# Performance work log

Hardware: AMD Instinct MI355X
Metric: run time of the kernel (lower is better)

## Reference

```python
import jax, jax.numpy as jnp
import numpy as np

B, S, D = 4, 2048, 1024
H, DK = 16, 64
NUM_BUCKETS = 32
MAX_DISTANCE = 128
EPS = 1e-6


def _relative_position_bucket(q_len, kv_len):
    # causal (bidirectional=False) T5 bucketization
    ctx = jnp.arange(q_len, dtype=jnp.int32)[:, None]
    mem = jnp.arange(kv_len, dtype=jnp.int32)[None, :]
    rp = mem - ctx                       # [q, kv]
    rp = -jnp.minimum(rp, 0)             # nonnegative distances to the past
    max_exact = NUM_BUCKETS // 2
    is_small = rp < max_exact
    rp_safe = jnp.maximum(rp, 1).astype(jnp.float32)
    large = max_exact + (
        jnp.log(rp_safe / max_exact) / np.log(MAX_DISTANCE / max_exact) * (NUM_BUCKETS - max_exact)
    ).astype(jnp.int32)
    large = jnp.minimum(large, NUM_BUCKETS - 1)
    return jnp.where(is_small, rp, large)  # [q, kv] int32 in [0, NUM_BUCKETS)


def setup_inputs() -> dict:
    key = jax.random.key(0)
    k1, k2, k3, k4 = jax.random.split(key, 4)
    hidden_states = jax.random.normal(k1, (B, S, D), dtype=jnp.float32)
    sequence_mask = jnp.ones((B, S), dtype=bool)
    rms_w = jnp.ones((D,), dtype=jnp.float32)
    W_qkv = jax.random.normal(k2, (D, 3 * H * DK), dtype=jnp.float32) * (D ** -0.5)
    W_o = jax.random.normal(k3, (H * DK, D), dtype=jnp.float32) * ((H * DK) ** -0.5)
    rel_bias = jax.random.normal(k4, (NUM_BUCKETS, H), dtype=jnp.float32)
    return {"hidden_states": hidden_states, "sequence_mask": sequence_mask,
            "rms_w": rms_w, "W_qkv": W_qkv, "W_o": W_o, "rel_bias": rel_bias}


def reference(hidden_states, sequence_mask, rms_w, W_qkv, W_o, rel_bias):
    # RMSNorm
    var = jnp.mean(hidden_states * hidden_states, axis=-1, keepdims=True)
    normed = hidden_states * jax.lax.rsqrt(var + EPS) * rms_w

    # QKV projection -> [B, S, 3, H, DK] -> [B, H, S, DK] each
    qkv = (normed @ W_qkv).reshape(B, S, 3, H, DK)
    q = jnp.transpose(qkv[:, :, 0], (0, 2, 1, 3))
    k = jnp.transpose(qkv[:, :, 1], (0, 2, 1, 3))
    v = jnp.transpose(qkv[:, :, 2], (0, 2, 1, 3))

    # relative position bias: gather [S,S,H] -> [1,H,S,S]
    bucket = _relative_position_bucket(S, S)
    pos_bias = jnp.transpose(rel_bias[bucket], (2, 0, 1))[None]

    # scores (note: T5 does NOT scale by 1/sqrt(dk))
    scores = jnp.einsum("bhqd,bhkd->bhqk", q, k) + pos_bias

    # causal mask combined with sequence mask (True = attend)
    causal = jnp.tril(jnp.ones((S, S), dtype=bool))
    mask = causal[None, None] & sequence_mask[:, None, None, :]
    scores = jnp.where(mask, scores, jnp.finfo(scores.dtype).min)

    attn = jax.nn.softmax(scores.astype(jnp.float32), axis=-1).astype(scores.dtype)
    # dropout p=0 / eval mode -> identity
    ctx = jnp.einsum("bhqk,bhkd->bhqd", attn, v)          # [B,H,S,DK]
    ctx = jnp.transpose(ctx, (0, 2, 1, 3)).reshape(B, S, H * DK)
    out = hidden_states + ctx @ W_o                        # residual
    return out
```

## Files before the change

### kernel.cpp

```cpp
#include <hip/hip_runtime.h>
#include <math.h>


typedef unsigned short ushort_t;
typedef __attribute__((ext_vector_type(8))) short bfrag;
typedef __attribute__((ext_vector_type(4))) float ffrag;

#define MFMA16(a, b, c) __builtin_amdgcn_mfma_f32_16x16x32_bf16((a), (b), (c), 0, 0, 0)

__device__ __forceinline__ void load_lds16(const ushort_t* g, ushort_t* l) {
  __builtin_amdgcn_global_load_lds(
      (const __attribute__((address_space(1))) unsigned int*)g,
      (__attribute__((address_space(3))) unsigned int*)l, 16, 0, 0);
}

__device__ __forceinline__ ushort_t f2bf(float f) {
  union { float f; unsigned u; } x; x.f = f;
  unsigned r = x.u + 0x7FFFu + ((x.u >> 16) & 1u);
  return (ushort_t)(r >> 16);
}
__device__ __forceinline__ float bf2f(ushort_t u) {
  union { unsigned u; float f; } x; x.u = ((unsigned)u) << 16; return x.f;
}
__device__ __forceinline__ unsigned pk2bf(float lo, float hi) {
  union { float f; unsigned u; } a, b; a.f = lo; b.f = hi;
  unsigned ra = a.u + 0x7FFFu + ((a.u >> 16) & 1u);
  unsigned rb = b.u + 0x7FFFu + ((b.u >> 16) & 1u);
  return (ra >> 16) | (rb & 0xFFFF0000u);
}

__global__ __launch_bounds__(256) void norm_cvt_kernel(
    const float* __restrict__ hidden, const float* __restrict__ rms_w,
    ushort_t* __restrict__ normed) {
  const int w = threadIdx.x >> 6, lane = threadIdx.x & 63;
  const int row = blockIdx.x * 4 + w;
  const float* p = hidden + (size_t)row * 1024;
  float4 v[4];
  float s = 0.f;
#pragma unroll
  for (int i = 0; i < 4; ++i) {
    v[i] = *(const float4*)(p + (lane + i * 64) * 4);
    s += v[i].x * v[i].x + v[i].y * v[i].y + v[i].z * v[i].z + v[i].w * v[i].w;
  }
#pragma unroll
  for (int off = 1; off < 64; off <<= 1) s += __shfl_xor(s, off, 64);
  const float scale = rsqrtf(s * (1.0f / 1024.0f) + 1e-6f);
#pragma unroll
  for (int i = 0; i < 4; ++i) {
    const int c0 = (lane + i * 64) * 4;
    float4 wv = *(const float4*)(rms_w + c0);
    ushort4 u;
    u.x = f2bf(v[i].x * scale * wv.x);
    u.y = f2bf(v[i].y * scale * wv.y);
    u.z = f2bf(v[i].z * scale * wv.z);
    u.w = f2bf(v[i].w * scale * wv.w);
    *(ushort4*)(normed + (size_t)row * 1024 + c0) = u;
  }
}

__global__ __launch_bounds__(256) void transpose_cvt_kernel(
    const float* __restrict__ in, ushort_t* __restrict__ out, int R, int C) {
  __shared__ float tile[32][33];
  const int r0 = blockIdx.y * 32, c0 = blockIdx.x * 32;
  const int tr = threadIdx.x >> 5, tc = threadIdx.x & 31;
#pragma unroll
  for (int i = 0; i < 32; i += 8)
    tile[tr + i][tc] = in[(size_t)(r0 + tr + i) * C + c0 + tc];
  __syncthreads();
#pragma unroll
  for (int i = 0; i < 32; i += 8)
    out[(size_t)(c0 + tr + i) * R + r0 + tc] = f2bf(tile[tc][tr + i]);
}

__global__ __launch_bounds__(256) void qkv_mfma_kernel(
    const ushort_t* __restrict__ A, const ushort_t* __restrict__ Bt,
    ushort_t* __restrict__ qbf, ushort_t* __restrict__ kbf,
    ushort_t* __restrict__ vtbf) {
  __shared__ ushort_t At[128 * 32];
  __shared__ ushort_t Bs[128 * 32];
  const int tid = threadIdx.x, w = tid >> 6, lane = tid & 63;
  const int quad = lane >> 4, ln = lane & 15;
  const int wr = w >> 1, wc = w & 1;
  const int m0 = blockIdx.y * 128, n0 = blockIdx.x * 128;
  const int srow = lane >> 2, scol = (lane & 3) * 8;

  ffrag acc[4][4];
#pragma unroll
  for (int i = 0; i < 4; ++i)
#pragma unroll
    for (int j = 0; j < 4; ++j) acc[i][j] = (ffrag)0.f;

  for (int kb = 0; kb < 1024; kb += 32) {
#pragma unroll
    for (int p = 0; p < 2; ++p) {
      load_lds16(A + (size_t)(m0 + (w * 2 + p) * 16 + srow) * 1024 + kb + scol,
                 At + (w * 2 + p) * 512);
      load_lds16(Bt + (size_t)(n0 + (w * 2 + p) * 16 + srow) * 1024 + kb + scol,
                 Bs + (w * 2 + p) * 512);
    }
    __syncthreads();
    bfrag a[4], b[4];
#pragma unroll
    for (int mi = 0; mi < 4; ++mi)
      a[mi] = *(const bfrag*)(At + (wr * 64 + mi * 16 + ln) * 32 + quad * 8);
#pragma unroll
    for (int ni = 0; ni < 4; ++ni)
      b[ni] = *(const bfrag*)(Bs + (wc * 64 + ni * 16 + ln) * 32 + quad * 8);
#pragma unroll
    for (int mi = 0; mi < 4; ++mi)
#pragma unroll
      for (int ni = 0; ni < 4; ++ni)
        acc[mi][ni] = MFMA16(a[mi], b[ni], acc[mi][ni]);
    __syncthreads();
  }

  const int b_idx = m0 >> 11;
  const int cbase = n0 + wc * 64 + ln;
#pragma unroll
  for (int mi = 0; mi < 4; ++mi) {
    const int sbase = (m0 & 2047) + wr * 64 + mi * 16 + quad * 4;
#pragma unroll
    for (int ni = 0; ni < 4; ++ni) {
      const int c = cbase + ni * 16;
      const int three = c >> 10, rem = c & 1023;
      const int h = rem >> 6, dk = rem & 63;
      if (three == 2) {
        ushort4 u;
        u.x = f2bf(acc[mi][ni][0]); u.y = f2bf(acc[mi][ni][1]);
        u.z = f2bf(acc[mi][ni][2]); u.w = f2bf(acc[mi][ni][3]);
        *(ushort4*)(vtbf + ((size_t)(b_idx * 16 + h) * 64 + dk) * 2048 + sbase) = u;
      } else {
        ushort_t* dst = (three == 0 ? qbf : kbf) +
                        ((size_t)(b_idx * 16 + h) * 2048 + sbase) * 64 + dk;
        dst[0]   = f2bf(acc[mi][ni][0]);
        dst[64]  = f2bf(acc[mi][ni][1]);
        dst[128] = f2bf(acc[mi][ni][2]);
        dst[192] = f2bf(acc[mi][ni][3]);
      }
    }
  }
}

__global__ __launch_bounds__(256) void attn_mfma_kernel(
    const ushort_t* __restrict__ qbf, const ushort_t* __restrict__ kbf,
    const ushort_t* __restrict__ vtbf, const float* __restrict__ rel_bias,
    ushort_t* __restrict__ ctx) {
  __shared__ ushort_t Kt[2][64][32];
  __shared__ ushort_t Vt[2][64][32];
  __shared__ ushort_t Pt[128][72];
  __shared__ ushort_t bias_t[2048];

  const int tid = threadIdx.x, w = tid >> 6, lane = tid & 63;
  const int quad = lane >> 4, ln = lane & 15;
  const int id = blockIdx.x;
  const int bh = id & 63;
  const int g = id >> 6;
  const int qb = (g < 4) ? (15 - 2 * g)
               : (g < 8) ? (2 * g - 8)
               : (g < 12) ? (30 - 2 * g)
                          : (2 * g - 23);
  const int h = bh & 15;

  for (int dist = tid; dist < 2048; dist += 256) {
    int bucket;
    if (dist < 16) bucket = dist;
    else {
      bucket = 16 + (int)(logf((float)dist * (1.0f / 16.0f)) * (16.0f / logf(8.0f)));
      if (bucket > 31) bucket = 31;
    }
    bias_t[dist] = f2bf(rel_bias[bucket * 16 + h]);
  }
  const float c31 = bf2f(f2bf(rel_bias[31 * 16 + h]));

  const int q0w = qb * 128 + w * 32;
  const size_t qrow = (size_t)bh * 2048 + q0w + ln;
  bfrag aq[2][2];
#pragma unroll
  for (int ni = 0; ni < 2; ++ni)
#pragma unroll
    for (int kf = 0; kf < 2; ++kf)
      aq[ni][kf] = *(const bfrag*)(qbf + (qrow + ni * 16) * 64 + kf * 32 + quad * 8);

  ffrag o[2][4];
  float m_run[2] = {-3.0e38f, -3.0e38f}, l_run[2] = {0.f, 0.f};
#pragma unroll
  for (int mo = 0; mo < 2; ++mo)
#pragma unroll
    for (int nd = 0; nd < 4; ++nd) o[mo][nd] = (ffrag)0.f;

  const int sidx = lane >> 2, scol8 = (lane & 3) * 8;
  const size_t khead = (size_t)bh * 2048 * 64;
  const int jmax = qb * 2 + 1;

  for (int j = 0; j <= jmax; ++j) {
    const int key0 = j * 64;
#pragma unroll
    for (int p = 0; p < 2; ++p) {
      const int idx = p * 4 + w, panel = idx >> 2, rb = idx & 3;
      load_lds16(kbf + khead + (size_t)(key0 + rb * 16 + sidx) * 64 + panel * 32 + scol8,
                 &Kt[0][0][0] + idx * 512);
      load_lds16(vtbf + khead + (size_t)(rb * 16 + sidx) * 2048 + key0 + panel * 32 + scol8,
                 &Vt[0][0][0] + idx * 512);
    }
    __syncthreads();

    if (key0 <= q0w + 31) {
      ffrag s[4][2];
#pragma unroll
      for (int mi = 0; mi < 4; ++mi)
#pragma unroll
        for (int ni = 0; ni < 2; ++ni) s[mi][ni] = (ffrag)0.f;
#pragma unroll
      for (int kf = 0; kf < 2; ++kf)
#pragma unroll
        for (int mi = 0; mi < 4; ++mi) {
          bfrag ak = *(const bfrag*)&Kt[kf][mi * 16 + ln][quad * 8];
          s[mi][0] = MFMA16(ak, aq[0][kf], s[mi][0]);
          s[mi][1] = MFMA16(ak, aq[1][kf], s[mi][1]);
        }

      float alpha[2];
      const bool fast = (key0 + 176 <= q0w);
      if (fast) {
#pragma unroll
        for (int ni = 0; ni < 2; ++ni) {
          float mx = s[0][ni][0];
#pragma unroll
          for (int mi = 0; mi < 4; ++mi)
#pragma unroll
            for (int r = 0; r < 4; ++r) mx = fmaxf(mx, s[mi][ni][r]);
          mx = fmaxf(mx, __shfl_xor(mx, 16, 64));
          mx = fmaxf(mx, __shfl_xor(mx, 32, 64));
          const float mnew = fmaxf(m_run[ni], mx + c31);
          alpha[ni] = __expf(m_run[ni] - mnew);
          const float sh = mnew - c31;
          float ps = 0.f;
#pragma unroll
          for (int mi = 0; mi < 4; ++mi)
#pragma unroll
            for (int r = 0; r < 4; ++r) {
              const float pv = __expf(s[mi][ni][r] - sh);
              s[mi][ni][r] = pv;
              ps += pv;
            }
          ps += __shfl_xor(ps, 16, 64);
          ps += __shfl_xor(ps, 32, 64);
          l_run[ni] = l_run[ni] * alpha[ni] + ps;
          m_run[ni] = mnew;
        }
      } else {
#pragma unroll
        for (int ni = 0; ni < 2; ++ni) {
          const int q = q0w + ni * 16 + ln;
          float mx = -3.0e38f;
#pragma unroll
          for (int mi = 0; mi < 4; ++mi) {
            const int keyb = key0 + mi * 16 + quad * 4;
#pragma unroll
            for (int r = 0; r < 4; ++r) {
              const int dist = q - (keyb + r);
              const float val =
                  (dist < 0) ? -3.0e38f : (s[mi][ni][r] + bf2f(bias_t[dist]));
              s[mi][ni][r] = val;
              mx = fmaxf(mx, val);
            }
          }
          mx = fmaxf(mx, __shfl_xor(mx, 16, 64));
          mx = fmaxf(mx, __shfl_xor(mx, 32, 64));
          const float mnew = fmaxf(m_run[ni], mx);
          alpha[ni] = __expf(m_run[ni] - mnew);
          float ps = 0.f;
#pragma unroll
          for (int mi = 0; mi < 4; ++mi)
#pragma unroll
            for (int r = 0; r < 4; ++r) {
              const float pv = __expf(s[mi][ni][r] - mnew);
              s[mi][ni][r] = pv;
              ps += pv;
            }
          ps += __shfl_xor(ps, 16, 64);
          ps += __shfl_xor(ps, 32, 64);
          l_run[ni] = l_run[ni] * alpha[ni] + ps;
          m_run[ni] = mnew;
        }
      }

#pragma unroll
      for (int ni = 0; ni < 2; ++ni) {
        ushort_t* prow = &Pt[w * 32 + ni * 16 + ln][0];
#pragma unroll
        for (int mi = 0; mi < 4; ++mi) {
          uint2 pk;
          pk.x = pk2bf(s[mi][ni][0], s[mi][ni][1]);
          pk.y = pk2bf(s[mi][ni][2], s[mi][ni][3]);
          *(uint2*)(prow + mi * 16 + quad * 4) = pk;
        }
      }

#pragma unroll
      for (int mo = 0; mo < 2; ++mo) {
#pragma unroll
        for (int r = 0; r < 4; ++r) {
          const float af = __shfl(alpha[mo], quad * 4 + r, 64);
#pragma unroll
          for (int nd = 0; nd < 4; ++nd) o[mo][nd][r] *= af;
        }
      }

#pragma unroll
      for (int kf = 0; kf < 2; ++kf) {
        bfrag ap0 = *(const bfrag*)&Pt[w * 32 + ln][kf * 32 + quad * 8];
        bfrag ap1 = *(const bfrag*)&Pt[w * 32 + 16 + ln][kf * 32 + quad * 8];
#pragma unroll
        for (int nd = 0; nd < 4; ++nd) {
          bfrag bv = *(const bfrag*)&Vt[kf][nd * 16 + ln][quad * 8];
          o[0][nd] = MFMA16(ap0, bv, o[0][nd]);
          o[1][nd] = MFMA16(ap1, bv, o[1][nd]);
        }
      }
    }
    __syncthreads();
  }

#pragma unroll
  for (int mo = 0; mo < 2; ++mo) {
    ffrag inv;
#pragma unroll
    for (int r = 0; r < 4; ++r)
      inv[r] = 1.0f / __shfl(l_run[mo], quad * 4 + r, 64);
    const int s0 = q0w + mo * 16 + quad * 4;
#pragma unroll
    for (int nd = 0; nd < 4; ++nd)
#pragma unroll
      for (int r = 0; r < 4; ++r)
        ctx[((size_t)(bh >> 4) * 2048 + s0 + r) * 1024 + h * 64 + nd * 16 + ln] =
            f2bf(o[mo][nd][r] * inv[r]);
  }
}

__global__ __launch_bounds__(256) void out_mfma_kernel(
    const ushort_t* __restrict__ A, const ushort_t* __restrict__ Bt,
    const float* __restrict__ hidden, float* __restrict__ out) {
  __shared__ ushort_t At[128 * 32];
  __shared__ ushort_t Bs[128 * 32];
  const int tid = threadIdx.x, w = tid >> 6, lane = tid & 63;
  const int quad = lane >> 4, ln = lane & 15;
  const int wr = w >> 1, wc = w & 1;
  const int m0 = blockIdx.y * 128, n0 = blockIdx.x * 128;
  const int srow = lane >> 2, scol = (lane & 3) * 8;

  ffrag acc[4][4];
#pragma unroll
  for (int i = 0; i < 4; ++i)
#pragma unroll
    for (int j = 0; j < 4; ++j) acc[i][j] = (ffrag)0.f;

  for (int kb = 0; kb < 1024; kb += 32) {
#pragma unroll
    for (int p = 0; p < 2; ++p) {
      load_lds16(A + (size_t)(m0 + (w * 2 + p) * 16 + srow) * 1024 + kb + scol,
                 At + (w * 2 + p) * 512);
      load_lds16(Bt + (size_t)(n0 + (w * 2 + p) * 16 + srow) * 1024 + kb + scol,
                 Bs + (w * 2 + p) * 512);
    }
    __syncthreads();
    bfrag a[4], b[4];
#pragma unroll
    for (int mi = 0; mi < 4; ++mi)
      a[mi] = *(const bfrag*)(At + (wr * 64 + mi * 16 + ln) * 32 + quad * 8);
#pragma unroll
    for (int ni = 0; ni < 4; ++ni)
      b[ni] = *(const bfrag*)(Bs + (wc * 64 + ni * 16 + ln) * 32 + quad * 8);
#pragma unroll
    for (int mi = 0; mi < 4; ++mi)
#pragma unroll
      for (int ni = 0; ni < 4; ++ni)
        acc[mi][ni] = MFMA16(a[mi], b[ni], acc[mi][ni]);
    __syncthreads();
  }
#pragma unroll
  for (int mi = 0; mi < 4; ++mi) {
    const int m = m0 + wr * 64 + mi * 16 + quad * 4;
#pragma unroll
    for (int ni = 0; ni < 4; ++ni) {
      const int c = n0 + wc * 64 + ni * 16 + ln;
#pragma unroll
      for (int r = 0; r < 4; ++r) {
        const size_t off = (size_t)(m + r) * 1024 + c;
        out[off] = acc[mi][ni][r] + hidden[off];
      }
    }
  }
}

extern "C" void kernel_launch(void* const* d_in, const int* in_sizes, int n_in,
                              void* d_out, int out_size, void* d_ws, size_t ws_size,
                              hipStream_t stream) {
  const size_t NORMED = (size_t)8192 * 1024;
  const size_t WQKVT  = (size_t)3072 * 1024;
  const size_t WOT    = (size_t)1024 * 1024;
  const size_t QKVE   = (size_t)64 * 2048 * 64;
  const size_t need = (NORMED + WQKVT + WOT + 3 * QKVE + NORMED) * 2;
  if (ws_size < need) return;

  const float* hidden   = (const float*)d_in[0];
  const float* rms_w    = (const float*)d_in[2];
  const float* Wqkv     = (const float*)d_in[3];
  const float* Wo       = (const float*)d_in[4];
  const float* rel_bias = (const float*)d_in[5];
  float* out = (float*)d_out;

  ushort_t* normed = (ushort_t*)d_ws;
  ushort_t* wqkvt  = normed + NORMED;
  ushort_t* wot    = wqkvt + WQKVT;
  ushort_t* qbf    = wot + WOT;
  ushort_t* kbf    = qbf + QKVE;
  ushort_t* vtbf   = kbf + QKVE;
  ushort_t* ctx    = vtbf + QKVE;

  norm_cvt_kernel<<<2048, 256, 0, stream>>>(hidden, rms_w, normed);
  transpose_cvt_kernel<<<dim3(96, 32), 256, 0, stream>>>(Wqkv, wqkvt, 1024, 3072);
  transpose_cvt_kernel<<<dim3(32, 32), 256, 0, stream>>>(Wo, wot, 1024, 1024);
  qkv_mfma_kernel<<<dim3(24, 64), 256, 0, stream>>>(normed, wqkvt, qbf, kbf, vtbf);
  attn_mfma_kernel<<<1024, 256, 0, stream>>>(qbf, kbf, vtbf, rel_bias, ctx);
  out_mfma_kernel<<<dim3(8, 64), 256, 0, stream>>>(ctx, wot, hidden, out);
}
```

Before: 308.0 us.

## Precompute fragment-layout bias tiles, fold log2e into K, use exp2 and fast bf16 rounding

A new small kernel precomputes the relative-position bias and causal mask for the near-diagonal tiles, already laid out in MFMA fragment order and scaled by log2(e). The attention kernel then drops its per-block LDS bias table and per-element distance/mask logic. K is pre-scaled by log2(e) in the QKV epilogue so softmax can use exp2f. Every bf16 conversion switches to a cheaper round-half-up (perm-based when packing), which slightly changes rounding versus round-to-nearest-even, and the extra launch and global bias reads add some cost.

New measurement: 327.8 us. 6.4% more time.

```diff
diff --git a/kernel.cpp b/kernel.cpp
--- a/kernel.cpp
+++ b/kernel.cpp
@@ -7,6 +7,7 @@
 typedef __attribute__((ext_vector_type(4))) float ffrag;
 
 #define MFMA16(a, b, c) __builtin_amdgcn_mfma_f32_16x16x32_bf16((a), (b), (c), 0, 0, 0)
+#define LOG2E 1.4426950408889634f
 
 __device__ __forceinline__ void load_lds16(const ushort_t* g, ushort_t* l) {
   __builtin_amdgcn_global_load_lds(
@@ -14,19 +15,45 @@
       (__attribute__((address_space(3))) unsigned int*)l, 16, 0, 0);
 }
 
-__device__ __forceinline__ ushort_t f2bf(float f) {
-  union { float f; unsigned u; } x; x.f = f;
-  unsigned r = x.u + 0x7FFFu + ((x.u >> 16) & 1u);
-  return (ushort_t)(r >> 16);
-}
-__device__ __forceinline__ float bf2f(ushort_t u) {
-  union { unsigned u; float f; } x; x.u = ((unsigned)u) << 16; return x.f;
-}
-__device__ __forceinline__ unsigned pk2bf(float lo, float hi) {
-  union { float f; unsigned u; } a, b; a.f = lo; b.f = hi;
-  unsigned ra = a.u + 0x7FFFu + ((a.u >> 16) & 1u);
-  unsigned rb = b.u + 0x7FFFu + ((b.u >> 16) & 1u);
-  return (ra >> 16) | (rb & 0xFFFF0000u);
+__device__ __forceinline__ ushort_t f2bf_fast(float f) {
+  return (ushort_t)((__float_as_uint(f) + 0x8000u) >> 16);
+}
+__device__ __forceinline__ unsigned pk2bf_fast(float lo, float hi) {
+  return __builtin_amdgcn_perm(__float_as_uint(hi) + 0x8000u,
+                               __float_as_uint(lo) + 0x8000u, 0x07060302u);
+}
+
+__global__ __launch_bounds__(64) void bias_precomp_kernel(
+    const float* __restrict__ rel_bias, float* __restrict__ bias_c) {
+  const int dlt = blockIdx.x;
+  const int h = blockIdx.y;
+  const int lane = threadIdx.x;
+  const int quad = lane >> 4, ln = lane & 15;
+  const int D = dlt * 32;
+  float vals[32];
+#pragma unroll
+  for (int mi = 0; mi < 4; ++mi)
+#pragma unroll
+    for (int ni = 0; ni < 2; ++ni)
+#pragma unroll
+      for (int r = 0; r < 4; ++r) {
+        const int dist = D + ni * 16 + ln - (mi * 16 + quad * 4 + r);
+        float v;
+        if (dist < 0) v = -3.0e38f;
+        else {
+          int bucket;
+          if (dist < 16) bucket = dist;
+          else {
+            bucket = 16 + (int)(logf((float)dist * (1.0f / 16.0f)) * (16.0f / logf(8.0f)));
+            if (bucket > 31) bucket = 31;
+          }
+          v = rel_bias[bucket * 16 + h] * LOG2E;
+        }
+        vals[mi * 8 + ni * 4 + r] = v;
+      }
+  float4* dst = (float4*)(bias_c + (((size_t)h * 6 + dlt) * 64 + lane) * 32);
+#pragma unroll
+  for (int i = 0; i < 8; ++i) dst[i] = ((float4*)vals)[i];
 }
 
 __global__ __launch_bounds__(256) void norm_cvt_kernel(
@@ -50,10 +77,10 @@
     const int c0 = (lane + i * 64) * 4;
     float4 wv = *(const float4*)(rms_w + c0);
     ushort4 u;
-    u.x = f2bf(v[i].x * scale * wv.x);
-    u.y = f2bf(v[i].y * scale * wv.y);
-    u.z = f2bf(v[i].z * scale * wv.z);
-    u.w = f2bf(v[i].w * scale * wv.w);
+    u.x = f2bf_fast(v[i].x * scale * wv.x);
+    u.y = f2bf_fast(v[i].y * scale * wv.y);
+    u.z = f2bf_fast(v[i].z * scale * wv.z);
+    u.w = f2bf_fast(v[i].w * scale * wv.w);
     *(ushort4*)(normed + (size_t)row * 1024 + c0) = u;
   }
 }
@@ -69,7 +96,7 @@
   __syncthreads();
 #pragma unroll
   for (int i = 0; i < 32; i += 8)
-    out[(size_t)(c0 + tr + i) * R + r0 + tc] = f2bf(tile[tc][tr + i]);
+    out[(size_t)(c0 + tr + i) * R + r0 + tc] = f2bf_fast(tile[tc][tr + i]);
 }
 
 __global__ __launch_bounds__(256) void qkv_mfma_kernel(
@@ -126,16 +153,17 @@
       const int h = rem >> 6, dk = rem & 63;
       if (three == 2) {
         ushort4 u;
-        u.x = f2bf(acc[mi][ni][0]); u.y = f2bf(acc[mi][ni][1]);
-        u.z = f2bf(acc[mi][ni][2]); u.w = f2bf(acc[mi][ni][3]);
+        u.x = f2bf_fast(acc[mi][ni][0]); u.y = f2bf_fast(acc[mi][ni][1]);
+        u.z = f2bf_fast(acc[mi][ni][2]); u.w = f2bf_fast(acc[mi][ni][3]);
         *(ushort4*)(vtbf + ((size_t)(b_idx * 16 + h) * 64 + dk) * 2048 + sbase) = u;
       } else {
+        const float kscale = (three == 1) ? LOG2E : 1.0f;
         ushort_t* dst = (three == 0 ? qbf : kbf) +
                         ((size_t)(b_idx * 16 + h) * 2048 + sbase) * 64 + dk;
-        dst[0]   = f2bf(acc[mi][ni][0]);
-        dst[64]  = f2bf(acc[mi][ni][1]);
-        dst[128] = f2bf(acc[mi][ni][2]);
-        dst[192] = f2bf(acc[mi][ni][3]);
+        dst[0]   = f2bf_fast(acc[mi][ni][0] * kscale);
+        dst[64]  = f2bf_fast(acc[mi][ni][1] * kscale);
+        dst[128] = f2bf_fast(acc[mi][ni][2] * kscale);
+        dst[192] = f2bf_fast(acc[mi][ni][3] * kscale);
       }
     }
   }
@@ -144,11 +172,10 @@
 __global__ __launch_bounds__(256) void attn_mfma_kernel(
     const ushort_t* __restrict__ qbf, const ushort_t* __restrict__ kbf,
     const ushort_t* __restrict__ vtbf, const float* __restrict__ rel_bias,
-    ushort_t* __restrict__ ctx) {
+    const float* __restrict__ bias_c, ushort_t* __restrict__ ctx) {
   __shared__ ushort_t Kt[2][64][32];
   __shared__ ushort_t Vt[2][64][32];
   __shared__ ushort_t Pt[128][72];
-  __shared__ ushort_t bias_t[2048];
 
   const int tid = threadIdx.x, w = tid >> 6, lane = tid & 63;
   const int quad = lane >> 4, ln = lane & 15;
@@ -160,17 +187,7 @@
                : (g < 12) ? (30 - 2 * g)
                           : (2 * g - 23);
   const int h = bh & 15;
-
-  for (int dist = tid; dist < 2048; dist += 256) {
-    int bucket;
-    if (dist < 16) bucket = dist;
-    else {
-      bucket = 16 + (int)(logf((float)dist * (1.0f / 16.0f)) * (16.0f / logf(8.0f)));
-      if (bucket > 31) bucket = 31;
-    }
-    bias_t[dist] = f2bf(rel_bias[bucket * 16 + h]);
-  }
-  const float c31 = bf2f(f2bf(rel_bias[31 * 16 + h]));
+  const float c31 = rel_bias[31 * 16 + h] * LOG2E;
 
   const int q0w = qb * 128 + w * 32;
   const size_t qrow = (size_t)bh * 2048 + q0w + ln;
@@ -232,14 +249,14 @@
           mx = fmaxf(mx, __shfl_xor(mx, 16, 64));
           mx = fmaxf(mx, __shfl_xor(mx, 32, 64));
           const float mnew = fmaxf(m_run[ni], mx + c31);
-          alpha[ni] = __expf(m_run[ni] - mnew);
+          alpha[ni] = exp2f(m_run[ni] - mnew);
           const float sh = mnew - c31;
           float ps = 0.f;
 #pragma unroll
           for (int mi = 0; mi < 4; ++mi)
 #pragma unroll
             for (int r = 0; r < 4; ++r) {
-              const float pv = __expf(s[mi][ni][r] - sh);
+              const float pv = exp2f(s[mi][ni][r] - sh);
               s[mi][ni][r] = pv;
               ps += pv;
             }
@@ -249,32 +266,33 @@
           m_run[ni] = mnew;
         }
       } else {
+        const float* bc =
+            bias_c + (((size_t)h * 6 + ((q0w - key0) >> 5)) * 64 + lane) * 32;
+        float mx[2] = {-3.0e38f, -3.0e38f};
+#pragma unroll
+        for (int mi = 0; mi < 4; ++mi) {
+          const float4 b0 = *(const float4*)(bc + mi * 8);
+          const float4 b1 = *(const float4*)(bc + mi * 8 + 4);
+#pragma unroll
+          for (int r = 0; r < 4; ++r) {
+            s[mi][0][r] += ((const float*)&b0)[r];
+            mx[0] = fmaxf(mx[0], s[mi][0][r]);
+            s[mi][1][r] += ((const float*)&b1)[r];
+            mx[1] = fmaxf(mx[1], s[mi][1][r]);
+          }
+        }
 #pragma unroll
         for (int ni = 0; ni < 2; ++ni) {
-          const int q = q0w + ni * 16 + ln;
-          float mx = -3.0e38f;
-#pragma unroll
-          for (int mi = 0; mi < 4; ++mi) {
-            const int keyb = key0 + mi * 16 + quad * 4;
+          float m2 = fmaxf(mx[ni], __shfl_xor(mx[ni], 16, 64));
+          m2 = fmaxf(m2, __shfl_xor(m2, 32, 64));
+          const float mnew = fmaxf(m_run[ni], m2);
+          alpha[ni] = exp2f(m_run[ni] - mnew);
+          float ps = 0.f;
+#pragma unroll
+          for (int mi = 0; mi < 4; ++mi)
 #pragma unroll
             for (int r = 0; r < 4; ++r) {
-              const int dist = q - (keyb + r);
-              const float val =
-                  (dist < 0) ? -3.0e38f : (s[mi][ni][r] + bf2f(bias_t[dist]));
-              s[mi][ni][r] = val;
-              mx = fmaxf(mx, val);
-            }
-          }
-          mx = fmaxf(mx, __shfl_xor(mx, 16, 64));
-          mx = fmaxf(mx, __shfl_xor(mx, 32, 64));
-          const float mnew = fmaxf(m_run[ni], mx);
-          alpha[ni] = __expf(m_run[ni] - mnew);
-          float ps = 0.f;
-#pragma unroll
-          for (int mi = 0; mi < 4; ++mi)
-#pragma unroll
-            for (int r = 0; r < 4; ++r) {
-              const float pv = __expf(s[mi][ni][r] - mnew);
+              const float pv = exp2f(s[mi][ni][r] - mnew);
               s[mi][ni][r] = pv;
               ps += pv;
             }
@@ -291,8 +309,8 @@
 #pragma unroll
         for (int mi = 0; mi < 4; ++mi) {
           uint2 pk;
-          pk.x = pk2bf(s[mi][ni][0], s[mi][ni][1]);
-          pk.y = pk2bf(s[mi][ni][2], s[mi][ni][3]);
+          pk.x = pk2bf_fast(s[mi][ni][0], s[mi][ni][1]);
+          pk.y = pk2bf_fast(s[mi][ni][2], s[mi][ni][3]);
           *(uint2*)(prow + mi * 16 + quad * 4) = pk;
         }
       }
@@ -334,7 +352,7 @@
 #pragma unroll
       for (int r = 0; r < 4; ++r)
         ctx[((size_t)(bh >> 4) * 2048 + s0 + r) * 1024 + h * 64 + nd * 16 + ln] =
-            f2bf(o[mo][nd][r] * inv[r]);
+            f2bf_fast(o[mo][nd][r] * inv[r]);
   }
 }
 
@@ -400,7 +418,9 @@
   const size_t WQKVT  = (size_t)3072 * 1024;
   const size_t WOT    = (size_t)1024 * 1024;
   const size_t QKVE   = (size_t)64 * 2048 * 64;
-  const size_t need = (NORMED + WQKVT + WOT + 3 * QKVE + NORMED) * 2;
+  const size_t USH    = NORMED + WQKVT + WOT + 3 * QKVE + NORMED;
+  const size_t BIASC  = (size_t)16 * 6 * 64 * 32;
+  const size_t need = USH * 2 + BIASC * 4;
   if (ws_size < need) return;
 
   const float* hidden   = (const float*)d_in[0];
@@ -417,11 +437,13 @@
   ushort_t* kbf    = qbf + QKVE;
   ushort_t* vtbf   = kbf + QKVE;
   ushort_t* ctx    = vtbf + QKVE;
-
+  float* bias_c    = (float*)(ctx + NORMED);
+
+  bias_precomp_kernel<<<dim3(6, 16), 64, 0, stream>>>(rel_bias, bias_c);
   norm_cvt_kernel<<<2048, 256, 0, stream>>>(hidden, rms_w, normed);
   transpose_cvt_kernel<<<dim3(96, 32), 256, 0, stream>>>(Wqkv, wqkvt, 1024, 3072);
   transpose_cvt_kernel<<<dim3(32, 32), 256, 0, stream>>>(Wo, wot, 1024, 1024);
   qkv_mfma_kernel<<<dim3(24, 64), 256, 0, stream>>>(normed, wqkvt, qbf, kbf, vtbf);
-  attn_mfma_kernel<<<1024, 256, 0, stream>>>(qbf, kbf, vtbf, rel_bias, ctx);
+  attn_mfma_kernel<<<1024, 256, 0, stream>>>(qbf, kbf, vtbf, rel_bias, bias_c, ctx);
   out_mfma_kernel<<<dim3(8, 64), 256, 0, stream>>>(ctx, wot, hidden, out);
 }
```
